# Optimization experiments

Measured on AMD Instinct MI355X. Metric: run time of the kernel, lower is better.

The kernel has to match this reference:

```python
import jax, jax.numpy as jnp
import numpy as np

N_HEADS = 8
N_LANDMARKS = 64
NEWTON_ITERS = 6


def _iterative_inv(mat):
    # mat: [B,H,L,L]; Newton-Schulz approximate inverse, 6 iterations
    L = mat.shape[-1]
    fro = jnp.sqrt(jnp.sum(mat * mat, axis=(-2, -1), keepdims=True))
    fro = jnp.maximum(fro, 1e-6)
    z = jnp.swapaxes(mat, -2, -1) / (fro * fro)
    for _ in range(NEWTON_ITERS):
        z = 2.0 * z - z @ mat @ z
    return z


def setup_inputs() -> dict:
    key = jax.random.key(0)
    ks = jax.random.split(key, 5)
    B, N, C = 4, 8192, 512
    s = 1.0 / np.sqrt(C)
    return {
        "x": jax.random.normal(ks[0], (B, N, C), jnp.float32),
        "Wqkv": jax.random.normal(ks[1], (3 * C, C), jnp.float32) * s,
        "bqkv": jax.random.normal(ks[2], (3 * C,), jnp.float32) * 0.01,
        "Wproj": jax.random.normal(ks[3], (C, C), jnp.float32) * s,
        "bproj": jax.random.normal(ks[4], (C,), jnp.float32) * 0.01,
    }


def reference(x, Wqkv, bqkv, Wproj, bproj):
    B, N, C = x.shape
    H = N_HEADS
    hd = C // H
    scale = hd ** (-0.5)
    n_lm = N_LANDMARKS

    qkv = x @ Wqkv.T + bqkv                       # [B,N,3C]
    qkv = qkv.reshape(B, N, 3, H, hd).transpose(2, 0, 3, 1, 4)  # [3,B,H,N,hd]
    q, k, v = qkv[0], qkv[1], qkv[2]

    if N <= n_lm:
        attn = jax.nn.softmax(q @ jnp.swapaxes(k, -2, -1) * scale, axis=-1)
        out = attn @ v
    else:
        stride = max(N // n_lm, 1)
        lm_idx = jnp.arange(0, N, stride)[:n_lm]
        q_lm = q[:, :, lm_idx]                    # [B,H,L,hd]
        k_lm = k[:, :, lm_idx]
        kernel_1 = jax.nn.softmax(q @ jnp.swapaxes(k_lm, -2, -1) * scale, axis=-1)   # [B,H,N,L]
        kernel_2 = jax.nn.softmax(q_lm @ jnp.swapaxes(k_lm, -2, -1) * scale, axis=-1)  # [B,H,L,L]
        kernel_3 = jax.nn.softmax(q_lm @ jnp.swapaxes(k, -2, -1) * scale, axis=-1)   # [B,H,L,N]
        kernel_2_inv = _iterative_inv(kernel_2)
        out = kernel_1 @ (kernel_2_inv @ (kernel_3 @ v))  # [B,H,N,hd]

    out = jnp.swapaxes(out, 1, 2).reshape(B, N, C)
    return out @ Wproj.T + bproj
```

## Files before the change

### kernel.cpp

```cpp
#include <hip/hip_runtime.h>

typedef unsigned short u16;
typedef unsigned int u32;

typedef __bf16 v8bf __attribute__((ext_vector_type(8)));
typedef float v4f __attribute__((ext_vector_type(4)));
typedef u16 v8u __attribute__((ext_vector_type(8)));

#define N_TOK 8192
#define CDIM 512
#define HEADS 8
#define HD 64
#define LM 64
#define LSTRIDE 128
#define BHN 32
#define NCHUNK 16
#define SCALE 0.125f

__device__ __forceinline__ float b2f(u16 u) { return __uint_as_float(((u32)u) << 16); }
__device__ __forceinline__ u16 f2bf(float f) {
  u32 u = __float_as_uint(f);
  u += 0x7fffu + ((u >> 16) & 1u);
  return (u16)(u >> 16);
}
__device__ __forceinline__ u32 pk2bf(float a, float b) {
  return (u32)f2bf(a) | ((u32)f2bf(b) << 16);
}

__global__ __launch_bounds__(256) void cast_bf16(const float* __restrict__ src,
                                                 u16* __restrict__ dst, int n8) {
  int i = blockIdx.x * 256 + threadIdx.x;
  if (i >= n8) return;
  const float4* s = (const float4*)src;
  float4 a = s[(size_t)i * 2], b = s[(size_t)i * 2 + 1];
  uint4 o;
  o.x = (u32)f2bf(a.x) | ((u32)f2bf(a.y) << 16);
  o.y = (u32)f2bf(a.z) | ((u32)f2bf(a.w) << 16);
  o.z = (u32)f2bf(b.x) | ((u32)f2bf(b.y) << 16);
  o.w = (u32)f2bf(b.z) | ((u32)f2bf(b.w) << 16);
  *(uint4*)(dst + (size_t)i * 8) = o;
}

template <int MODE>
__global__ __launch_bounds__(256) void gemm_bt(const u16* __restrict__ A,
                                               const u16* __restrict__ Bm,
                                               const float* __restrict__ bias,
                                               u16* __restrict__ qo,
                                               u16* __restrict__ ko,
                                               u16* __restrict__ vo,
                                               float* __restrict__ outp) {
  __shared__ u16 As[128 * 40];
  __shared__ u16 Bs[128 * 40];
  const int K = 512;
  const int m0 = blockIdx.x * 128;
  const int n0 = blockIdx.y * 128;
  const int t = threadIdx.x;
  const int lane = t & 63, w = t >> 6;
  const int wm = w >> 1, wn = w & 1;
  const int quad = lane >> 4, lrow = lane & 15;

  v4f acc[4][4];
#pragma unroll
  for (int i = 0; i < 4; ++i)
#pragma unroll
    for (int j = 0; j < 4; ++j)
#pragma unroll
      for (int r = 0; r < 4; ++r) acc[i][j][r] = 0.f;

  for (int kt = 0; kt < K; kt += 32) {
    __syncthreads();
#pragma unroll
    for (int p = 0; p < 2; ++p) {
      int lin = p * 256 + t;
      int row = lin >> 2, c8 = (lin & 3) * 8;
      *(uint4*)&As[row * 40 + c8] = *(const uint4*)(A + (size_t)(m0 + row) * K + kt + c8);
      *(uint4*)&Bs[row * 40 + c8] = *(const uint4*)(Bm + (size_t)(n0 + row) * K + kt + c8);
    }
    __syncthreads();
    v8bf af[4], bf[4];
#pragma unroll
    for (int ti = 0; ti < 4; ++ti)
      af[ti] = *(const v8bf*)&As[(wm * 64 + ti * 16 + lrow) * 40 + quad * 8];
#pragma unroll
    for (int tj = 0; tj < 4; ++tj)
      bf[tj] = *(const v8bf*)&Bs[(wn * 64 + tj * 16 + lrow) * 40 + quad * 8];
#pragma unroll
    for (int ti = 0; ti < 4; ++ti)
#pragma unroll
      for (int tj = 0; tj < 4; ++tj)
        acc[ti][tj] = __builtin_amdgcn_mfma_f32_16x16x32_bf16(af[ti], bf[tj], acc[ti][tj], 0, 0, 0);
  }

#pragma unroll
  for (int ti = 0; ti < 4; ++ti) {
#pragma unroll
    for (int tj = 0; tj < 4; ++tj) {
      int gn = n0 + wn * 64 + tj * 16 + lrow;
      float bv = bias[gn];
#pragma unroll
      for (int r = 0; r < 4; ++r) {
        int gm = m0 + wm * 64 + ti * 16 + quad * 4 + r;
        float val = acc[ti][tj][r] + bv;
        if (MODE == 0) {
          int tt = gn >> 9;
          int h = (gn >> 6) & 7;
          int d = gn & 63;
          int b = gm >> 13;
          int n = gm & 8191;
          size_t di = ((size_t)(b * HEADS + h) * N_TOK + n) * HD + d;
          u16* dst = (tt == 0) ? qo : (tt == 1) ? ko : vo;
          dst[di] = f2bf(val);
        } else {
          outp[(size_t)gm * CDIM + gn] = val;
        }
      }
    }
  }
}

__global__ __launch_bounds__(256) void fpart(const u16* __restrict__ qb,
                                             const u16* __restrict__ kb,
                                             const u16* __restrict__ vb,
                                             float* __restrict__ Fp,
                                             float* __restrict__ Mc,
                                             float* __restrict__ Sc) {
  __shared__ __align__(16) char smem[4 * 64 * 40 * 2 * 2];
  __shared__ float msh[4][64], ssh[4][64];
  const int jc = blockIdx.x, bh = blockIdx.y;
  const int t = threadIdx.x;
  const int lane = t & 63, w = t >> 6;
  const int col = lane & 15, quad = lane >> 4;
  const int jq = lane & 7, dh = lane >> 3;

  u16* Pw = (u16*)smem + w * (64 * 40);
  u16* vT = (u16*)smem + 4 * (64 * 40) + w * (64 * 40);
  float* Fbuf = (float*)smem;

  v8bf qf[4][2];
#pragma unroll
  for (int it = 0; it < 4; ++it)
#pragma unroll
    for (int kh = 0; kh < 2; ++kh)
      qf[it][kh] = *(const v8bf*)(qb + ((size_t)bh * N_TOK + (size_t)(it * 16 + col) * LSTRIDE) * HD + kh * 32 + quad * 8);

  float mw[4], sw[4];
  v4f facc[4][4];
#pragma unroll
  for (int it = 0; it < 4; ++it) { mw[it] = -3.0e38f; sw[it] = 0.f; }
#pragma unroll
  for (int dt = 0; dt < 4; ++dt)
#pragma unroll
    for (int it = 0; it < 4; ++it)
#pragma unroll
      for (int r = 0; r < 4; ++r) facc[dt][it][r] = 0.f;

  for (int st = 0; st < 4; ++st) {
    const int j0 = jc * 512 + w * 128 + st * 32;

    v8bf kf[2][2];
#pragma unroll
    for (int jt = 0; jt < 2; ++jt)
#pragma unroll
      for (int kh = 0; kh < 2; ++kh)
        kf[jt][kh] = *(const v8bf*)(kb + ((size_t)bh * N_TOK + j0 + jt * 16 + col) * HD + kh * 32 + quad * 8);

    v8u r0 = *(const v8u*)(vb + ((size_t)bh * N_TOK + j0 + jq * 4 + 0) * HD + dh * 8);
    v8u r1 = *(const v8u*)(vb + ((size_t)bh * N_TOK + j0 + jq * 4 + 1) * HD + dh * 8);
    v8u r2 = *(const v8u*)(vb + ((size_t)bh * N_TOK + j0 + jq * 4 + 2) * HD + dh * 8);
    v8u r3 = *(const v8u*)(vb + ((size_t)bh * N_TOK + j0 + jq * 4 + 3) * HD + dh * 8);
#pragma unroll
    for (int e = 0; e < 8; ++e) {
      uint2 pk;
      pk.x = (u32)r0[e] | ((u32)r1[e] << 16);
      pk.y = (u32)r2[e] | ((u32)r3[e] << 16);
      *(uint2*)&vT[(dh * 8 + e) * 40 + jq * 4] = pk;
    }

    v4f sacc[2][4];
#pragma unroll
    for (int jt = 0; jt < 2; ++jt)
#pragma unroll
      for (int it = 0; it < 4; ++it) {
#pragma unroll
        for (int r = 0; r < 4; ++r) sacc[jt][it][r] = 0.f;
#pragma unroll
        for (int kh = 0; kh < 2; ++kh)
          sacc[jt][it] = __builtin_amdgcn_mfma_f32_16x16x32_bf16(kf[jt][kh], qf[it][kh], sacc[jt][it], 0, 0, 0);
      }

#pragma unroll
    for (int it = 0; it < 4; ++it) {
      float mloc = -3.0e38f;
#pragma unroll
      for (int jt = 0; jt < 2; ++jt)
#pragma unroll
        for (int r = 0; r < 4; ++r) {
          float s = sacc[jt][it][r] * SCALE;
          sacc[jt][it][r] = s;
          mloc = fmaxf(mloc, s);
        }
      mloc = fmaxf(mloc, __shfl_xor(mloc, 16));
      mloc = fmaxf(mloc, __shfl_xor(mloc, 32));
      float mnew = fmaxf(mw[it], mloc);
      float alpha = __expf(mw[it] - mnew);
      mw[it] = mnew;
      float rs = 0.f;
#pragma unroll
      for (int jt = 0; jt < 2; ++jt)
#pragma unroll
        for (int r = 0; r < 4; ++r) {
          float p = __expf(sacc[jt][it][r] - mnew);
          sacc[jt][it][r] = p;
          rs += p;
        }
      rs += __shfl_xor(rs, 16);
      rs += __shfl_xor(rs, 32);
      sw[it] = sw[it] * alpha + rs;
#pragma unroll
      for (int jt = 0; jt < 2; ++jt) {
        uint2 pk;
        pk.x = pk2bf(sacc[jt][it][0], sacc[jt][it][1]);
        pk.y = pk2bf(sacc[jt][it][2], sacc[jt][it][3]);
        *(uint2*)&Pw[(it * 16 + col) * 40 + jt * 16 + quad * 4] = pk;
      }
#pragma unroll
      for (int dt = 0; dt < 4; ++dt)
#pragma unroll
        for (int r = 0; r < 4; ++r) facc[dt][it][r] *= alpha;
    }

    v8bf vfr[4], pfr[4];
#pragma unroll
    for (int dt = 0; dt < 4; ++dt)
      vfr[dt] = *(const v8bf*)&vT[(dt * 16 + col) * 40 + quad * 8];
#pragma unroll
    for (int it = 0; it < 4; ++it)
      pfr[it] = *(const v8bf*)&Pw[(it * 16 + col) * 40 + quad * 8];
#pragma unroll
    for (int dt = 0; dt < 4; ++dt)
#pragma unroll
      for (int it = 0; it < 4; ++it)
        facc[dt][it] = __builtin_amdgcn_mfma_f32_16x16x32_bf16(vfr[dt], pfr[it], facc[dt][it], 0, 0, 0);
  }

  if (quad == 0) {
#pragma unroll
    for (int it = 0; it < 4; ++it) {
      msh[w][it * 16 + col] = mw[it];
      ssh[w][it * 16 + col] = sw[it];
    }
  }
  __syncthreads();

  const size_t cb = (size_t)(bh * NCHUNK + jc) * 64;
  float scl[4];
#pragma unroll
  for (int it = 0; it < 4; ++it) {
    int i = it * 16 + col;
    float m0 = msh[0][i], m1 = msh[1][i], m2 = msh[2][i], m3 = msh[3][i];
    float M = fmaxf(fmaxf(m0, m1), fmaxf(m2, m3));
    float e0 = __expf(m0 - M), e1 = __expf(m1 - M);
    float e2 = __expf(m2 - M), e3 = __expf(m3 - M);
    float Stot = e0 * ssh[0][i] + e1 * ssh[1][i] + e2 * ssh[2][i] + e3 * ssh[3][i];
    scl[it] = (w == 0) ? e0 : (w == 1) ? e1 : (w == 2) ? e2 : e3;
    if (w == 0 && quad == 0) {
      Mc[cb + i] = M;
      Sc[cb + i] = Stot;
    }
  }

  for (int wv = 0; wv < 4; ++wv) {
    if (w == wv) {
#pragma unroll
      for (int it = 0; it < 4; ++it)
#pragma unroll
        for (int dt = 0; dt < 4; ++dt) {
          float* dst = &Fbuf[(it * 16 + col) * 76 + dt * 16 + quad * 4];
          float4 v;
          v.x = facc[dt][it][0] * scl[it];
          v.y = facc[dt][it][1] * scl[it];
          v.z = facc[dt][it][2] * scl[it];
          v.w = facc[dt][it][3] * scl[it];
          if (wv == 0) {
            *(float4*)dst = v;
          } else {
            float4 o = *(float4*)dst;
            o.x += v.x; o.y += v.y; o.z += v.z; o.w += v.w;
            *(float4*)dst = o;
          }
        }
    }
    __syncthreads();
  }

  size_t base = (size_t)(bh * NCHUNK + jc) * 4096;
#pragma unroll
  for (int p = 0; p < 16; ++p) {
    int idx = p * 256 + t;
    Fp[base + idx] = Fbuf[(idx >> 6) * 76 + (idx & 63)];
  }
}

__global__ __launch_bounds__(256) void newton_t(const u16* __restrict__ qb,
                                                const u16* __restrict__ kb,
                                                const float* __restrict__ Fp,
                                                const float* __restrict__ Mc,
                                                const float* __restrict__ Sc,
                                                u16* __restrict__ Tt) {
  __shared__ float Ms[4096];
  __shared__ float Z0s[4096];
  __shared__ float Ws[4096];
  __shared__ float Xs[4096];
  const int bh = blockIdx.x;
  const int t = threadIdx.x;
  const int lane = t & 63, w = t >> 6;
  const int ti = t >> 4, tj = t & 15;

#pragma unroll
  for (int p = 0; p < 16; ++p) {
    int idx = p * 256 + t;
    int i = idx >> 6, d = idx & 63;
    Ws[idx] = b2f(qb[((size_t)bh * N_TOK + i * LSTRIDE) * HD + d]);
    Xs[d * 64 + i] = b2f(kb[((size_t)bh * N_TOK + i * LSTRIDE) * HD + d]);
  }
  __syncthreads();

  {
    float a2[4][4];
#pragma unroll
    for (int a = 0; a < 4; ++a)
#pragma unroll
      for (int b = 0; b < 4; ++b) a2[a][b] = 0.f;
    for (int d = 0; d < 64; ++d) {
      float qa[4], kv[4];
#pragma unroll
      for (int a = 0; a < 4; ++a) qa[a] = Ws[(ti * 4 + a) * 64 + d];
#pragma unroll
      for (int b = 0; b < 4; ++b) kv[b] = Xs[d * 64 + tj * 4 + b];
#pragma unroll
      for (int a = 0; a < 4; ++a)
#pragma unroll
        for (int b = 0; b < 4; ++b) a2[a][b] += qa[a] * kv[b];
    }
    __syncthreads();
#pragma unroll
    for (int a = 0; a < 4; ++a)
#pragma unroll
      for (int b = 0; b < 4; ++b) Ms[(ti * 4 + a) * 64 + tj * 4 + b] = a2[a][b] * SCALE;
  }
  __syncthreads();

  for (int rr = 0; rr < 16; ++rr) {
    int i = w * 16 + rr;
    float vv = Ms[i * 64 + lane];
    float m = vv;
#pragma unroll
    for (int off = 32; off; off >>= 1) m = fmaxf(m, __shfl_xor(m, off));
    float e = expf(vv - m);
    float s = e;
#pragma unroll
    for (int off = 32; off; off >>= 1) s += __shfl_xor(s, off);
    Ms[i * 64 + lane] = e / s;
  }
  __syncthreads();

  float loc = 0.f;
#pragma unroll
  for (int p = 0; p < 16; ++p) {
    float v = Ms[p * 256 + t];
    loc += v * v;
  }
#pragma unroll
  for (int off = 32; off; off >>= 1) loc += __shfl_xor(loc, off);
  if (lane == 0) Z0s[w] = loc;
  __syncthreads();
  float fro = fmaxf(sqrtf(Z0s[0] + Z0s[1] + Z0s[2] + Z0s[3]), 1e-6f);
  float invden = 1.0f / (fro * fro);
  __syncthreads();

#pragma unroll
  for (int p = 0; p < 16; ++p) {
    int idx = p * 256 + t;
    int i = idx >> 6, j = idx & 63;
    Z0s[j * 64 + i] = Ms[idx] * invden;
  }
  __syncthreads();

  float* Z = Z0s;
  float* Zn = Xs;
  for (int it = 0; it < 6; ++it) {
    {
      float a2[4][4];
#pragma unroll
      for (int a = 0; a < 4; ++a)
#pragma unroll
        for (int b = 0; b < 4; ++b) a2[a][b] = 0.f;
      for (int tt = 0; tt < 64; ++tt) {
        float za[4], mb[4];
#pragma unroll
        for (int a = 0; a < 4; ++a) za[a] = Z[(ti * 4 + a) * 64 + tt];
#pragma unroll
        for (int b = 0; b < 4; ++b) mb[b] = Ms[tt * 64 + tj * 4 + b];
#pragma unroll
        for (int a = 0; a < 4; ++a)
#pragma unroll
          for (int b = 0; b < 4; ++b) a2[a][b] += za[a] * mb[b];
      }
#pragma unroll
      for (int a = 0; a < 4; ++a)
#pragma unroll
        for (int b = 0; b < 4; ++b) Ws[(ti * 4 + a) * 64 + tj * 4 + b] = a2[a][b];
    }
    __syncthreads();
    {
      float a2[4][4];
#pragma unroll
      for (int a = 0; a < 4; ++a)
#pragma unroll
        for (int b = 0; b < 4; ++b) a2[a][b] = 0.f;
      for (int tt = 0; tt < 64; ++tt) {
        float wa[4], zb[4];
#pragma unroll
        for (int a = 0; a < 4; ++a) wa[a] = Ws[(ti * 4 + a) * 64 + tt];
#pragma unroll
        for (int b = 0; b < 4; ++b) zb[b] = Z[tt * 64 + tj * 4 + b];
#pragma unroll
        for (int a = 0; a < 4; ++a)
#pragma unroll
          for (int b = 0; b < 4; ++b) a2[a][b] += wa[a] * zb[b];
      }
#pragma unroll
      for (int a = 0; a < 4; ++a)
#pragma unroll
        for (int b = 0; b < 4; ++b)
          Zn[(ti * 4 + a) * 64 + tj * 4 + b] =
              2.f * Z[(ti * 4 + a) * 64 + tj * 4 + b] - a2[a][b];
    }
    __syncthreads();
    float* tmp = Z; Z = Zn; Zn = tmp;
  }

  float* wts = Ms;
  if (t < 64) {
    float M = -3.0e38f;
#pragma unroll
    for (int jc = 0; jc < NCHUNK; ++jc)
      M = fmaxf(M, Mc[(bh * NCHUNK + jc) * 64 + t]);
    float S = 0.f;
#pragma unroll
    for (int jc = 0; jc < NCHUNK; ++jc)
      S += expf(Mc[(bh * NCHUNK + jc) * 64 + t] - M) * Sc[(bh * NCHUNK + jc) * 64 + t];
    float invS = 1.0f / S;
#pragma unroll
    for (int jc = 0; jc < NCHUNK; ++jc)
      wts[jc * 64 + t] = expf(Mc[(bh * NCHUNK + jc) * 64 + t] - M) * invS;
  }
  __syncthreads();

#pragma unroll
  for (int p = 0; p < 16; ++p) {
    int idx = p * 256 + t;
    int i = idx >> 6;
    float sum = 0.f;
#pragma unroll
    for (int jc = 0; jc < NCHUNK; ++jc)
      sum += wts[jc * 64 + i] * Fp[(size_t)(bh * NCHUNK + jc) * 4096 + idx];
    Ws[idx] = sum;
  }
  __syncthreads();

  {
    float a2[4][4];
#pragma unroll
    for (int a = 0; a < 4; ++a)
#pragma unroll
      for (int b = 0; b < 4; ++b) a2[a][b] = 0.f;
    for (int tt = 0; tt < 64; ++tt) {
      float za[4], fb[4];
#pragma unroll
      for (int a = 0; a < 4; ++a) za[a] = Z[(ti * 4 + a) * 64 + tt];
#pragma unroll
      for (int b = 0; b < 4; ++b) fb[b] = Ws[tt * 64 + tj * 4 + b];
#pragma unroll
      for (int a = 0; a < 4; ++a)
#pragma unroll
        for (int b = 0; b < 4; ++b) a2[a][b] += za[a] * fb[b];
    }
#pragma unroll
    for (int a = 0; a < 4; ++a)
#pragma unroll
      for (int b = 0; b < 4; ++b)
        Tt[(size_t)bh * 4096 + (size_t)(tj * 4 + b) * 64 + (ti * 4 + a)] = f2bf(a2[a][b]);
  }
}

__global__ __launch_bounds__(256) void attn_out_k(const u16* __restrict__ qb,
                                                  const u16* __restrict__ kb,
                                                  const u16* __restrict__ Tt,
                                                  u16* __restrict__ ao) {
  __shared__ __align__(16) u16 Pl[4][1024];
  const int bh = blockIdx.y;
  const int b = bh >> 3, h = bh & 7;
  const int t = threadIdx.x;
  const int lane = t & 63, w = t >> 6;
  const int col = lane & 15, quad = lane >> 4;
  const int rot = (col & 7) * 8;

  v8bf kfr[4][2], tfr[4][2];
#pragma unroll
  for (int tj = 0; tj < 4; ++tj)
#pragma unroll
    for (int kh = 0; kh < 2; ++kh)
      kfr[tj][kh] = *(const v8bf*)(kb + ((size_t)bh * N_TOK + (size_t)(tj * 16 + col) * LSTRIDE) * HD + kh * 32 + quad * 8);
#pragma unroll
  for (int td = 0; td < 4; ++td)
#pragma unroll
    for (int jh = 0; jh < 2; ++jh)
      tfr[td][jh] = *(const v8bf*)(Tt + (size_t)bh * 4096 + (size_t)(td * 16 + col) * 64 + jh * 32 + quad * 8);

  u16* Pw = &Pl[w][0];

  for (int tile = 0; tile < 4; ++tile) {
    const int n0 = blockIdx.x * 256 + w * 64 + tile * 16;
    v8bf qf[2];
#pragma unroll
    for (int kh = 0; kh < 2; ++kh)
      qf[kh] = *(const v8bf*)(qb + ((size_t)bh * N_TOK + n0 + col) * HD + kh * 32 + quad * 8);

    v4f S[4];
#pragma unroll
    for (int tj = 0; tj < 4; ++tj) {
#pragma unroll
      for (int r = 0; r < 4; ++r) S[tj][r] = 0.f;
#pragma unroll
      for (int kh = 0; kh < 2; ++kh)
        S[tj] = __builtin_amdgcn_mfma_f32_16x16x32_bf16(kfr[tj][kh], qf[kh], S[tj], 0, 0, 0);
    }

    float mx = -3.0e38f;
#pragma unroll
    for (int tj = 0; tj < 4; ++tj)
#pragma unroll
      for (int r = 0; r < 4; ++r) {
        S[tj][r] *= SCALE;
        mx = fmaxf(mx, S[tj][r]);
      }
    mx = fmaxf(mx, __shfl_xor(mx, 16));
    mx = fmaxf(mx, __shfl_xor(mx, 32));
    float sum = 0.f;
#pragma unroll
    for (int tj = 0; tj < 4; ++tj)
#pragma unroll
      for (int r = 0; r < 4; ++r) {
        S[tj][r] = __expf(S[tj][r] - mx);
        sum += S[tj][r];
      }
    sum += __shfl_xor(sum, 16);
    sum += __shfl_xor(sum, 32);
    float inv = 1.0f / sum;

#pragma unroll
    for (int tj = 0; tj < 4; ++tj) {
      u32 lo = (u32)f2bf(S[tj][0] * inv) | ((u32)f2bf(S[tj][1] * inv) << 16);
      u32 hi = (u32)f2bf(S[tj][2] * inv) | ((u32)f2bf(S[tj][3] * inv) << 16);
      uint2 pk = {lo, hi};
      *(uint2*)&Pw[col * 64 + ((tj * 16 + quad * 4 + rot) & 63)] = pk;
    }
    v8bf pf[2];
#pragma unroll
    for (int jh = 0; jh < 2; ++jh)
      pf[jh] = *(const v8bf*)&Pw[col * 64 + ((jh * 32 + quad * 8 + rot) & 63)];

    v4f O[4];
#pragma unroll
    for (int td = 0; td < 4; ++td) {
#pragma unroll
      for (int r = 0; r < 4; ++r) O[td][r] = 0.f;
#pragma unroll
      for (int jh = 0; jh < 2; ++jh)
        O[td] = __builtin_amdgcn_mfma_f32_16x16x32_bf16(pf[jh], tfr[td][jh], O[td], 0, 0, 0);
    }
#pragma unroll
    for (int td = 0; td < 4; ++td)
#pragma unroll
      for (int r = 0; r < 4; ++r) {
        int n = n0 + quad * 4 + r;
        ao[((size_t)(b * N_TOK + n)) * CDIM + h * HD + td * 16 + col] = f2bf(O[td][r]);
      }
  }
}

__global__ void ws_too_small_sentinel(float* out) {
  if (threadIdx.x == 0 && blockIdx.x == 0) out[0] = 1.0f;
}

static constexpr size_t SZ_QKV = (size_t)BHN * N_TOK * HD * 2;
static constexpr size_t OFF_Q = 0;
static constexpr size_t OFF_K = OFF_Q + SZ_QKV;
static constexpr size_t OFF_V = OFF_K + SZ_QKV;
static constexpr size_t OFF_FP = OFF_V + SZ_QKV;
static constexpr size_t SZ_FP = (size_t)BHN * NCHUNK * 4096 * 4;
static constexpr size_t OFF_MC = OFF_FP + SZ_FP;
static constexpr size_t SZ_MS = (size_t)BHN * NCHUNK * 64 * 4;
static constexpr size_t OFF_SC = OFF_MC + SZ_MS;
static constexpr size_t OFF_T = OFF_SC + SZ_MS;
static constexpr size_t OFF_WQ = OFF_T + (size_t)BHN * 4096 * 2;
static constexpr size_t OFF_WP = OFF_WQ + (size_t)3 * CDIM * CDIM * 2;
static constexpr size_t OFF_END = OFF_WP + (size_t)CDIM * CDIM * 2;

extern "C" void kernel_launch(void* const* d_in, const int* in_sizes, int n_in,
                              void* d_out, int out_size, void* d_ws, size_t ws_size,
                              hipStream_t stream) {
  const float* x = (const float*)d_in[0];
  const float* Wqkv = (const float*)d_in[1];
  const float* bqkv = (const float*)d_in[2];
  const float* Wproj = (const float*)d_in[3];
  const float* bproj = (const float*)d_in[4];
  float* out = (float*)d_out;
  char* ws = (char*)d_ws;
  if (ws_size < OFF_END) {
    ws_too_small_sentinel<<<1, 64, 0, stream>>>(out);
    return;
  }

  u16* qb = (u16*)(ws + OFF_Q);
  u16* kb = (u16*)(ws + OFF_K);
  u16* vb = (u16*)(ws + OFF_V);
  float* Fp = (float*)(ws + OFF_FP);
  float* Mc = (float*)(ws + OFF_MC);
  float* Sc = (float*)(ws + OFF_SC);
  u16* Tt = (u16*)(ws + OFF_T);
  u16* Wqb = (u16*)(ws + OFF_WQ);
  u16* Wpb = (u16*)(ws + OFF_WP);
  u16* attn = (u16*)(ws + OFF_V);
  u16* xb = (u16*)d_out;

  cast_bf16<<<8192, 256, 0, stream>>>(x, xb, 2097152);
  cast_bf16<<<384, 256, 0, stream>>>(Wqkv, Wqb, 98304);
  cast_bf16<<<128, 256, 0, stream>>>(Wproj, Wpb, 32768);
  gemm_bt<0><<<dim3(256, 12), 256, 0, stream>>>(xb, Wqb, bqkv, qb, kb, vb, nullptr);
  fpart<<<dim3(NCHUNK, BHN), 256, 0, stream>>>(qb, kb, vb, Fp, Mc, Sc);
  newton_t<<<dim3(BHN), 256, 0, stream>>>(qb, kb, Fp, Mc, Sc, Tt);
  attn_out_k<<<dim3(32, BHN), 256, 0, stream>>>(qb, kb, Tt, attn);
  gemm_bt<1><<<dim3(256, 4), 256, 0, stream>>>(attn, Wpb, bproj, nullptr, nullptr, nullptr, out);
}
```

Measured before the change: 339.6 us.

## Rewrite bf16 GEMM with 256x256 tiles, direct global-to-LDS loads, and pipelining

Replaces the 128x128 synchronous-load GEMM with a 512-thread, 256x256-tile kernel. It uses global_load_lds to copy straight into a double-buffered, XOR-swizzled shared memory layout, and interleaves staged prefetches with MFMA phases under explicit barriers and priority hints. The aim is to hide global latency, remove register staging and bank conflicts, and raise data reuse per tile. The cost is 64 KB of LDS and many accumulator registers per block. The projection GEMM now launches only 256 blocks, which may underfill the GPU.

```diff
diff --git a/kernel.cpp b/kernel.cpp
--- a/kernel.cpp
+++ b/kernel.cpp
@@ -25,6 +25,12 @@
 }
 __device__ __forceinline__ u32 pk2bf(float a, float b) {
   return (u32)f2bf(a) | ((u32)f2bf(b) << 16);
+}
+
+__device__ __forceinline__ void gl_lds16(const u16* g, u16* l) {
+  __builtin_amdgcn_global_load_lds(
+      (const __attribute__((address_space(1))) u32*)g,
+      (__attribute__((address_space(3))) u32*)l, 16, 0, 0);
 }
 
 __global__ __launch_bounds__(256) void cast_bf16(const float* __restrict__ src,
@@ -42,65 +48,132 @@
 }
 
 template <int MODE>
-__global__ __launch_bounds__(256) void gemm_bt(const u16* __restrict__ A,
+__global__ __launch_bounds__(512) void gemm_bt(const u16* __restrict__ A,
                                                const u16* __restrict__ Bm,
                                                const float* __restrict__ bias,
                                                u16* __restrict__ qo,
                                                u16* __restrict__ ko,
                                                u16* __restrict__ vo,
                                                float* __restrict__ outp) {
-  __shared__ u16 As[128 * 40];
-  __shared__ u16 Bs[128 * 40];
+  __shared__ __align__(16) u16 Al[16384];
+  __shared__ __align__(16) u16 Bl[16384];
   const int K = 512;
-  const int m0 = blockIdx.x * 128;
-  const int n0 = blockIdx.y * 128;
+  const int NT = 16;
+  const int m0 = blockIdx.x * 256;
+  const int n0 = blockIdx.y * 256;
   const int t = threadIdx.x;
   const int lane = t & 63, w = t >> 6;
-  const int wm = w >> 1, wn = w & 1;
+  const int wm = w >> 2, wn = w & 3;
   const int quad = lane >> 4, lrow = lane & 15;
-
-  v4f acc[4][4];
-#pragma unroll
-  for (int i = 0; i < 4; ++i)
+  const int rslot = (quad ^ ((lrow >> 1) & 3)) * 8;
+
+  const int srl = t >> 2, slt = t & 3;
+  const int gch = (slt ^ ((srl >> 1) & 3)) * 8;
+  const int rA0 = ((srl >> 6) & 1) * 128 + (srl & 63);
+  const int rB0 = ((srl >> 5) & 3) * 64 + (srl & 31);
+
+#define STAGE_A(tt, qg, bb)                                                  \
+  gl_lds16(A + (size_t)(m0 + rA0 + (qg) * 64) * K + (tt) * 32 + gch,         \
+           &Al[(bb) * 8192 + (qg) * 4096 + t * 8])
+#define STAGE_B(tt, qg, bb)                                                  \
+  gl_lds16(Bm + (size_t)(n0 + rB0 + (qg) * 32) * K + (tt) * 32 + gch,        \
+           &Bl[(bb) * 8192 + (qg) * 4096 + t * 8])
+
+  v4f acc[8][4];
+#pragma unroll
+  for (int i = 0; i < 8; ++i)
 #pragma unroll
     for (int j = 0; j < 4; ++j)
 #pragma unroll
       for (int r = 0; r < 4; ++r) acc[i][j][r] = 0.f;
 
-  for (int kt = 0; kt < K; kt += 32) {
-    __syncthreads();
-#pragma unroll
-    for (int p = 0; p < 2; ++p) {
-      int lin = p * 256 + t;
-      int row = lin >> 2, c8 = (lin & 3) * 8;
-      *(uint4*)&As[row * 40 + c8] = *(const uint4*)(A + (size_t)(m0 + row) * K + kt + c8);
-      *(uint4*)&Bs[row * 40 + c8] = *(const uint4*)(Bm + (size_t)(n0 + row) * K + kt + c8);
-    }
-    __syncthreads();
-    v8bf af[4], bf[4];
-#pragma unroll
-    for (int ti = 0; ti < 4; ++ti)
-      af[ti] = *(const v8bf*)&As[(wm * 64 + ti * 16 + lrow) * 40 + quad * 8];
-#pragma unroll
-    for (int tj = 0; tj < 4; ++tj)
-      bf[tj] = *(const v8bf*)&Bs[(wn * 64 + tj * 16 + lrow) * 40 + quad * 8];
-#pragma unroll
-    for (int ti = 0; ti < 4; ++ti)
-#pragma unroll
-      for (int tj = 0; tj < 4; ++tj)
-        acc[ti][tj] = __builtin_amdgcn_mfma_f32_16x16x32_bf16(af[ti], bf[tj], acc[ti][tj], 0, 0, 0);
-  }
-
-#pragma unroll
-  for (int ti = 0; ti < 4; ++ti) {
-#pragma unroll
-    for (int tj = 0; tj < 4; ++tj) {
-      int gn = n0 + wn * 64 + tj * 16 + lrow;
+  STAGE_A(0, 0, 0); STAGE_B(0, 0, 0);
+  STAGE_A(0, 1, 0); STAGE_B(0, 1, 0);
+  STAGE_A(1, 0, 1); STAGE_B(1, 0, 1);
+
+  v8bf af[4], b0[2], b1[2];
+#pragma unroll 2
+  for (int u = 0; u < NT; ++u) {
+    const int bu = u & 1, bn = bu ^ 1;
+    const u16* Ab = &Al[bu * 8192];
+    const u16* Bb = &Bl[bu * 8192];
+    asm volatile("s_waitcnt vmcnt(2)" ::: "memory");
+    __builtin_amdgcn_s_barrier();
+    __builtin_amdgcn_sched_barrier(0);
+#pragma unroll
+    for (int ml = 0; ml < 4; ++ml)
+      af[ml] = *(const v8bf*)&Ab[(wm * 64 + ml * 16 + lrow) * 32 + rslot];
+#pragma unroll
+    for (int nl = 0; nl < 2; ++nl)
+      b0[nl] = *(const v8bf*)&Bb[(wn * 32 + nl * 16 + lrow) * 32 + rslot];
+    if (u + 1 < NT) STAGE_A(u + 1, 1, bn);
+    __builtin_amdgcn_sched_barrier(0);
+    __builtin_amdgcn_s_barrier();
+    __builtin_amdgcn_sched_barrier(0);
+    __builtin_amdgcn_s_setprio(1);
+#pragma unroll
+    for (int ml = 0; ml < 4; ++ml)
+#pragma unroll
+      for (int nl = 0; nl < 2; ++nl)
+        acc[ml][nl] = __builtin_amdgcn_mfma_f32_16x16x32_bf16(af[ml], b0[nl], acc[ml][nl], 0, 0, 0);
+    __builtin_amdgcn_s_setprio(0);
+    __builtin_amdgcn_s_barrier();
+#pragma unroll
+    for (int nl = 0; nl < 2; ++nl)
+      b1[nl] = *(const v8bf*)&Bb[4096 + (wn * 32 + nl * 16 + lrow) * 32 + rslot];
+    if (u + 1 < NT) STAGE_B(u + 1, 1, bn);
+    __builtin_amdgcn_sched_barrier(0);
+    __builtin_amdgcn_s_barrier();
+    __builtin_amdgcn_sched_barrier(0);
+    __builtin_amdgcn_s_setprio(1);
+#pragma unroll
+    for (int ml = 0; ml < 4; ++ml)
+#pragma unroll
+      for (int nl = 0; nl < 2; ++nl)
+        acc[ml][2 + nl] = __builtin_amdgcn_mfma_f32_16x16x32_bf16(af[ml], b1[nl], acc[ml][2 + nl], 0, 0, 0);
+    __builtin_amdgcn_s_setprio(0);
+    __builtin_amdgcn_s_barrier();
+#pragma unroll
+    for (int ml = 0; ml < 4; ++ml)
+      af[ml] = *(const v8bf*)&Ab[4096 + (wm * 64 + ml * 16 + lrow) * 32 + rslot];
+    if (u + 2 < NT) STAGE_A(u + 2, 0, bu);
+    __builtin_amdgcn_sched_barrier(0);
+    __builtin_amdgcn_s_barrier();
+    __builtin_amdgcn_sched_barrier(0);
+    __builtin_amdgcn_s_setprio(1);
+#pragma unroll
+    for (int ml = 0; ml < 4; ++ml)
+#pragma unroll
+      for (int nl = 0; nl < 2; ++nl)
+        acc[4 + ml][nl] = __builtin_amdgcn_mfma_f32_16x16x32_bf16(af[ml], b0[nl], acc[4 + ml][nl], 0, 0, 0);
+    __builtin_amdgcn_s_setprio(0);
+    __builtin_amdgcn_s_barrier();
+    if (u + 2 < NT) STAGE_B(u + 2, 0, bu);
+    __builtin_amdgcn_sched_barrier(0);
+    __builtin_amdgcn_s_barrier();
+    __builtin_amdgcn_sched_barrier(0);
+    __builtin_amdgcn_s_setprio(1);
+#pragma unroll
+    for (int ml = 0; ml < 4; ++ml)
+#pragma unroll
+      for (int nl = 0; nl < 2; ++nl)
+        acc[4 + ml][2 + nl] = __builtin_amdgcn_mfma_f32_16x16x32_bf16(af[ml], b1[nl], acc[4 + ml][2 + nl], 0, 0, 0);
+    __builtin_amdgcn_s_setprio(0);
+    __builtin_amdgcn_s_barrier();
+  }
+#undef STAGE_A
+#undef STAGE_B
+
+#pragma unroll
+  for (int mf = 0; mf < 8; ++mf) {
+#pragma unroll
+    for (int nf = 0; nf < 4; ++nf) {
+      int gn = n0 + wn * 64 + nf * 16 + lrow;
       float bv = bias[gn];
 #pragma unroll
       for (int r = 0; r < 4; ++r) {
-        int gm = m0 + wm * 64 + ti * 16 + quad * 4 + r;
-        float val = acc[ti][tj][r] + bv;
+        int gm = m0 + wm * 128 + mf * 16 + quad * 4 + r;
+        float val = acc[mf][nf][r] + bv;
         if (MODE == 0) {
           int tt = gn >> 9;
           int h = (gn >> 6) & 7;
@@ -638,9 +711,9 @@
   cast_bf16<<<8192, 256, 0, stream>>>(x, xb, 2097152);
   cast_bf16<<<384, 256, 0, stream>>>(Wqkv, Wqb, 98304);
   cast_bf16<<<128, 256, 0, stream>>>(Wproj, Wpb, 32768);
-  gemm_bt<0><<<dim3(256, 12), 256, 0, stream>>>(xb, Wqb, bqkv, qb, kb, vb, nullptr);
+  gemm_bt<0><<<dim3(128, 6), 512, 0, stream>>>(xb, Wqb, bqkv, qb, kb, vb, nullptr);
   fpart<<<dim3(NCHUNK, BHN), 256, 0, stream>>>(qb, kb, vb, Fp, Mc, Sc);
   newton_t<<<dim3(BHN), 256, 0, stream>>>(qb, kb, Fp, Mc, Sc, Tt);
   attn_out_k<<<dim3(32, BHN), 256, 0, stream>>>(qb, kb, Tt, attn);
-  gemm_bt<1><<<dim3(256, 4), 256, 0, stream>>>(attn, Wpb, bproj, nullptr, nullptr, nullptr, out);
-}
+  gemm_bt<1><<<dim3(128, 2), 512, 0, stream>>>(attn, Wpb, bproj, nullptr, nullptr, nullptr, out);
+}
```

Measured after the change: 313.1 us. 7.8% less time.
